# Performance work log

Hardware: AMD Instinct MI355X
Metric: run time of the kernel (lower is better)

## Reference

```python
import jax, jax.numpy as jnp
import numpy as np

N = 131072        # total points
M = 34            # max_num_neighbors (hard-coded in forward)
K = 15            # kernel points (torch-points3d default for 3D KPConv)
C_IN, C_OUT = 32, 64
POINT_INFLUENCE = 0.04        # prev_grid_size * sigma
KERNEL_RADIUS = 1.5 * POINT_INFLUENCE  # _INFLUENCE_TO_RADIUS * point_influence
BN_EPS = 1e-5
NEG_SLOPE = 0.2


def setup_inputs() -> dict:
    key = jax.random.key(0)
    ks = jax.random.split(key, 6)
    # points in a [0, 0.1]^3 box so random neighbors can fall inside the influence radius
    xyz = jax.random.uniform(ks[0], (N, 3), jnp.float32) * 0.1
    feats = jax.random.normal(ks[1], (N, C_IN), jnp.float32)
    neighbor_idx = jax.random.randint(ks[2], (N, M), 0, N, dtype=jnp.int32)
    # fixed kernel-point disposition: points inside a sphere of radius KERNEL_RADIUS
    kp_dir = jax.random.normal(ks[3], (K, 3), jnp.float32)
    kp_dir = kp_dir / jnp.linalg.norm(kp_dir, axis=1, keepdims=True)
    kp_rad = jax.random.uniform(ks[4], (K, 1), jnp.float32) ** (1.0 / 3.0)
    k_points = kp_dir * kp_rad * KERNEL_RADIUS
    weight = jax.random.normal(ks[5], (K, C_IN, C_OUT), jnp.float32) / np.sqrt(K * C_IN)
    gamma = jnp.ones((C_OUT,), jnp.float32)
    beta = jnp.zeros((C_OUT,), jnp.float32)
    return {"xyz": xyz, "feats": feats, "neighbor_idx": neighbor_idx,
            "weight": weight, "k_points": k_points, "gamma": gamma, "beta": beta}


def _kpconv(xyz, feats, neighbor_idx, weight, k_points):
    # shadow point / shadow feature row for out-of-range neighbor index == N
    sup = jnp.concatenate([xyz, jnp.full((1, 3), 1e6, xyz.dtype)], axis=0)
    f = jnp.concatenate([feats, jnp.zeros((1, feats.shape[1]), feats.dtype)], axis=0)
    # [N, M, 3] neighbor offsets relative to each query point
    nb = sup[neighbor_idx] - xyz[:, None, :]
    # [N, M, K] distance from each neighbor to each kernel point
    diff = nb[:, :, None, :] - k_points[None, None, :, :]
    dist = jnp.sqrt(jnp.sum(diff * diff, axis=-1))
    # linear kernel influence, 'sum' aggregation
    w = jnp.maximum(0.0, 1.0 - dist / POINT_INFLUENCE)          # [N, M, K]
    nb_f = f[neighbor_idx]                                       # [N, M, C_IN]
    wf = jnp.einsum('nmk,nmc->nkc', w, nb_f)                     # [N, K, C_IN]
    return jnp.einsum('nkc,kcd->nd', wf, weight)                 # [N, C_OUT]


def reference(xyz, feats, neighbor_idx, weight, k_points, gamma, beta):
    out = _kpconv(xyz, feats, neighbor_idx, weight, k_points)
    # FastBatchNorm1d (training-mode batch statistics) + LeakyReLU(0.2)
    mean = jnp.mean(out, axis=0)
    var = jnp.mean((out - mean) ** 2, axis=0)
    out = (out - mean) * jax.lax.rsqrt(var + BN_EPS) * gamma + beta
    return jnp.where(out >= 0, out, NEG_SLOPE * out)
```

## Files before the change

kernel.cpp:

```cpp
#include <hip/hip_runtime.h>

#define NPTS 131072
#define MNBR 34
#define KP 15
#define CIN 32
#define COUT 64
#define INV_INFL 25.0f
#define BN_EPS 1e-5f
#define NEG_SLOPE 0.2f
#define PPB 16
#define NBLK (NPTS / PPB)
#define NBIN 512

typedef unsigned short u16;
typedef unsigned int u32;
typedef short short8 __attribute__((ext_vector_type(8)));
typedef float f32x4 __attribute__((ext_vector_type(4)));

static __device__ __forceinline__ u16 f2bf(float f) {
    u32 x = __float_as_uint(f);
    x += 0x7fffu + ((x >> 16) & 1u);
    return (u16)(x >> 16);
}
static __device__ __forceinline__ u32 pk2bf(float lo, float hi) {
    u32 a = __float_as_uint(lo) + 0x8000u;
    u32 b = __float_as_uint(hi) + 0x8000u;
    return (a >> 16) | (b & 0xffff0000u);
}

#define WS_WT   0u
#define WS_SCSH 65536u
#define WS_SP   131072u
#define WS_QP   262144u
#define WS_XY   393216u
#define WS_FB   2490624u

__global__ __launch_bounds__(256) void prep(const float* __restrict__ Wg,
                                            const float* __restrict__ feats,
                                            const float* __restrict__ xyz,
                                            u16* __restrict__ WT, float4* __restrict__ XY,
                                            u32* __restrict__ FBu, float* __restrict__ SpQp) {
    int b = blockIdx.x;
    if (b < 120) {
        int i2 = b * 256 + threadIdx.x;
        WT[(i2 & 63) * 480 + (i2 >> 6)] = f2bf(Wg[i2]);
    } else if (b < 633) {
        int r = (b - 120) * 256 + threadIdx.x;
        if (r <= NPTS) {
            float4 v;
            if (r < NPTS) v = make_float4(xyz[3 * r], xyz[3 * r + 1], xyz[3 * r + 2], 0.f);
            else          v = make_float4(1e6f, 1e6f, 1e6f, 0.f);
            XY[r] = v;
        }
    } else if (b < 8826) {
        int g = (b - 633) * 256 + threadIdx.x;
        if (g < ((NPTS + 1) * CIN) / 2) {
            int e = g * 2;
            u32 v = 0;
            if (e < NPTS * CIN)
                v = (u32)f2bf(feats[e]) | ((u32)f2bf(feats[e + 1]) << 16);
            FBu[g] = v;
        }
    } else {
        SpQp[(b - 8826) * 256 + threadIdx.x] = 0.f;
    }
}

__global__ __launch_bounds__(128, 3) void kpconv_conv(
    const float* __restrict__ xyz, const int* __restrict__ nbr,
    const float4* __restrict__ XY, const u32* __restrict__ FBu,
    const u16* __restrict__ WT, const float* __restrict__ kpts,
    float* __restrict__ out, float* __restrict__ Sp, float* __restrict__ Qp)
{
    __shared__ u32 wf[PPB * 256];
    __shared__ float4 offs4[2][2][64];
    __shared__ u32 idxs[2][2][64];

    const int tid = threadIdx.x, lane = tid & 63, wave = tid >> 6;
    const int q = lane >> 4, t = lane & 15;
    const int pbase = blockIdx.x * PPB + wave * 8;

    float axt = 0.f, ayt = 0.f, azt = 0.f, ckt = 1e30f;
    if (t < KP) {
        float kx = kpts[3 * t], ky = kpts[3 * t + 1], kz = kpts[3 * t + 2];
        axt = -2.f * kx; ayt = -2.f * ky; azt = -2.f * kz;
        ckt = fmaf(kx, kx, fmaf(ky, ky, kz * kz));
    }
    const int wslot = (lane & ~7) | ((lane ^ (lane >> 3)) & 7);

    auto ldnbr = [&](int pp) {
        int v = NPTS;
        if (lane < MNBR) v = nbr[(size_t)(pbase + pp) * MNBR + lane];
        if ((u32)v > (u32)NPTS) v = NPTS;
        return v;
    };

    u32 fbC[8], fbN[8] = {0,0,0,0,0,0,0,0};
    u32 d32C = 0, d33C = 0, d32N = 0, d33N = 0;

    int ixA = ldnbr(0);
    int ix1 = ldnbr(1);
    int ix2 = ldnbr(2);
    float4 pn0 = XY[ixA];
    float4 pn1 = XY[ix1];
    {
        const int n1 = pbase;
        float qx = xyz[3 * n1], qy = xyz[3 * n1 + 1], qz = xyz[3 * n1 + 2];
        float ox = pn0.x - qx, oy = pn0.y - qy, oz = pn0.z - qz;
        offs4[wave][0][wslot] = make_float4(ox, oy, oz, fmaf(ox, ox, fmaf(oy, oy, oz * oz)));
        idxs[wave][0][lane] = (u32)ixA;
        #pragma unroll
        for (int j = 0; j < 8; ++j) {
            u32 row = idxs[wave][0][q * 8 + j];
            fbC[j] = FBu[(size_t)row * 16 + t];
        }
        int r32 = __builtin_amdgcn_readlane(ixA, 32);
        int r33 = __builtin_amdgcn_readlane(ixA, 33);
        d32C = FBu[(size_t)r32 * 16 + t];
        d33C = FBu[(size_t)r33 * 16 + t];
    }

    for (int p = 0; p < 8; ++p) {
        int ixN = NPTS;
        if (p < 5) ixN = ldnbr(p + 3);
        float4 pn2 = make_float4(1e6f, 1e6f, 1e6f, 0.f);
        if (p < 6) pn2 = XY[ix2];
        if (p < 7) {
            const int n1 = pbase + p + 1;
            float qx = xyz[3 * n1], qy = xyz[3 * n1 + 1], qz = xyz[3 * n1 + 2];
            float ox = pn1.x - qx, oy = pn1.y - qy, oz = pn1.z - qz;
            const int bb = (p + 1) & 1;
            offs4[wave][bb][wslot] = make_float4(ox, oy, oz, fmaf(ox, ox, fmaf(oy, oy, oz * oz)));
            idxs[wave][bb][lane] = (u32)ix1;
            #pragma unroll
            for (int j = 0; j < 8; ++j) {
                u32 row = idxs[wave][bb][q * 8 + j];
                fbN[j] = FBu[(size_t)row * 16 + t];
            }
            int r32 = __builtin_amdgcn_readlane(ix1, 32);
            int r33 = __builtin_amdgcn_readlane(ix1, 33);
            d32N = FBu[(size_t)r32 * 16 + t];
            d33N = FBu[(size_t)r33 * 16 + t];
        }

        const float4* ob = &offs4[wave][p & 1][0];
        float wj[8];
        #pragma unroll
        for (int j = 0; j < 8; ++j) {
            float4 o = ob[q * 8 + (j ^ q)];
            float d2 = fmaf(o.x, axt, fmaf(o.y, ayt, fmaf(o.z, azt, ckt))) + o.w;
            float dd = __builtin_amdgcn_sqrtf(d2);
            wj[j] = fmaxf(0.f, fmaf(dd, -INV_INFL, 1.f));
        }
        union { short8 v; u32 d[4]; } a1, a2, e1, o1, e2, o2;
        #pragma unroll
        for (int i = 0; i < 4; ++i) a1.d[i] = pk2bf(wj[2 * i], wj[2 * i + 1]);
        {
            float4 oA = ob[36], oB = ob[37];
            float dA = __builtin_amdgcn_sqrtf(fmaf(oA.x, axt, fmaf(oA.y, ayt, fmaf(oA.z, azt, ckt))) + oA.w);
            float dB = __builtin_amdgcn_sqrtf(fmaf(oB.x, axt, fmaf(oB.y, ayt, fmaf(oB.z, azt, ckt))) + oB.w);
            float wA = fmaxf(0.f, fmaf(dA, -INV_INFL, 1.f));
            float wB = fmaxf(0.f, fmaf(dB, -INV_INFL, 1.f));
            a2.d[0] = (q == 0) ? pk2bf(wA, wB) : 0u;
            a2.d[1] = 0; a2.d[2] = 0; a2.d[3] = 0;
        }
        #pragma unroll
        for (int i = 0; i < 4; ++i) {
            u32 aa = fbC[2 * i], bb2 = fbC[2 * i + 1];
            e1.d[i] = (aa & 0xffffu) | (bb2 << 16);
            o1.d[i] = (aa >> 16) | (bb2 & 0xffff0000u);
        }
        {
            u32 lo = (d32C & 0xffffu) | (d33C << 16);
            u32 hi = (d32C >> 16) | (d33C & 0xffff0000u);
            e2.d[0] = (q == 0) ? lo : 0u;  e2.d[1] = 0; e2.d[2] = 0; e2.d[3] = 0;
            o2.d[0] = (q == 0) ? hi : 0u;  o2.d[1] = 0; o2.d[2] = 0; o2.d[3] = 0;
        }
        f32x4 c0 = {0.f, 0.f, 0.f, 0.f}, c1 = {0.f, 0.f, 0.f, 0.f};
        c0 = __builtin_amdgcn_mfma_f32_16x16x32_bf16(a1.v, e1.v, c0, 0, 0, 0);
        c0 = __builtin_amdgcn_mfma_f32_16x16x32_bf16(a2.v, e2.v, c0, 0, 0, 0);
        c1 = __builtin_amdgcn_mfma_f32_16x16x32_bf16(a1.v, o1.v, c1, 0, 0, 0);
        c1 = __builtin_amdgcn_mfma_f32_16x16x32_bf16(a2.v, o2.v, c1, 0, 0, 0);

        const int row = wave * 8 + p;
        #pragma unroll
        for (int r = 0; r < 4; ++r) {
            int ko = q * 4 + r;
            u32 pk = pk2bf(c0[r], c1[r]);
            int unit = ko * 4 + (t >> 2);
            wf[row * 256 + ((unit ^ (row & 7)) << 2) + (t & 3)] = pk;
        }

        #pragma unroll
        for (int j = 0; j < 8; ++j) fbC[j] = fbN[j];
        d32C = d32N; d33C = d33N;
        pn1 = pn2; ix1 = ix2; ix2 = ixN;
    }
    __syncthreads();

    const int wcol0 = (wave * 2 + 0) * 16 + t;
    const int wcol1 = (wave * 2 + 1) * 16 + t;
    f32x4 A0 = {0.f, 0.f, 0.f, 0.f}, A1 = {0.f, 0.f, 0.f, 0.f};
    const u16* wt0 = WT + wcol0 * 480 + q * 8;
    const u16* wt1 = WT + wcol1 * 480 + q * 8;
    #pragma unroll
    for (int ks = 0; ks < KP; ++ks) {
        const int u = ks * 4 + q;
        short8 a   = *(const short8*)&wf[t * 256 + ((u ^ (t & 7)) << 2)];
        short8 bb0 = *(const short8*)(wt0 + ks * 32);
        short8 bb1 = *(const short8*)(wt1 + ks * 32);
        A0 = __builtin_amdgcn_mfma_f32_16x16x32_bf16(a, bb0, A0, 0, 0, 0);
        A1 = __builtin_amdgcn_mfma_f32_16x16x32_bf16(a, bb1, A1, 0, 0, 0);
    }
    const int base = blockIdx.x * PPB;
    float s0 = 0.f, q0 = 0.f, s1 = 0.f, q1 = 0.f;
    #pragma unroll
    for (int r = 0; r < 4; ++r) {
        float v0 = A0[r], v1 = A1[r];
        out[(base + q * 4 + r) * COUT + wcol0] = v0;
        out[(base + q * 4 + r) * COUT + wcol1] = v1;
        s0 += v0; q0 = fmaf(v0, v0, q0);
        s1 += v1; q1 = fmaf(v1, v1, q1);
    }
    s0 += __shfl_xor(s0, 16, 64); s0 += __shfl_xor(s0, 32, 64);
    q0 += __shfl_xor(q0, 16, 64); q0 += __shfl_xor(q0, 32, 64);
    s1 += __shfl_xor(s1, 16, 64); s1 += __shfl_xor(s1, 32, 64);
    q1 += __shfl_xor(q1, 16, 64); q1 += __shfl_xor(q1, 32, 64);
    if (q == 0) {
        const int bin = blockIdx.x >> 4;
        atomicAdd(&Sp[wcol0 * NBIN + bin], s0);
        atomicAdd(&Qp[wcol0 * NBIN + bin], q0);
        atomicAdd(&Sp[wcol1 * NBIN + bin], s1);
        atomicAdd(&Qp[wcol1 * NBIN + bin], q1);
    }
}

__global__ __launch_bounds__(256) void bn_reduce(
    const float* __restrict__ Sp, const float* __restrict__ Qp,
    const float* __restrict__ gamma, const float* __restrict__ beta,
    float* __restrict__ scsh)
{
    const int ch = blockIdx.x;
    const int tid = threadIdx.x;
    float s = 0.f, qq = 0.f;
    if (tid < NBIN / 4) {
        float4 a = ((const float4*)(Sp + ch * NBIN))[tid]; s  = a.x + a.y + a.z + a.w;
        float4 b = ((const float4*)(Qp + ch * NBIN))[tid]; qq = b.x + b.y + b.z + b.w;
    }
    #pragma unroll
    for (int off = 1; off < 64; off <<= 1) {
        s += __shfl_xor(s, off, 64); qq += __shfl_xor(qq, off, 64);
    }
    __shared__ float red[8];
    const int w = tid >> 6;
    if ((tid & 63) == 0) { red[w * 2] = s; red[w * 2 + 1] = qq; }
    __syncthreads();
    if (tid == 0) {
        s  = red[0] + red[2] + red[4] + red[6];
        qq = red[1] + red[3] + red[5] + red[7];
        float mean = s * (1.0f / NPTS);
        float var  = qq * (1.0f / NPTS) - mean * mean;
        float sc = gamma[ch] * rsqrtf(var + BN_EPS);
        scsh[ch] = sc;
        scsh[64 + ch] = beta[ch] - mean * sc;
    }
}

__global__ __launch_bounds__(256) void bn_apply(
    float* __restrict__ out, const float* __restrict__ scsh)
{
    __shared__ float sc[64], sh[64];
    const int tid = threadIdx.x;
    if (tid < 64) { sc[tid] = scsh[tid]; sh[tid] = scsh[64 + tid]; }
    __syncthreads();
    const int gid = blockIdx.x * 256 + tid;
    float4 v = ((const float4*)out)[gid];
    const int c0 = (gid * 4) & 63;
    float y0 = fmaf(v.x, sc[c0 + 0], sh[c0 + 0]);
    float y1 = fmaf(v.y, sc[c0 + 1], sh[c0 + 1]);
    float y2 = fmaf(v.z, sc[c0 + 2], sh[c0 + 2]);
    float y3 = fmaf(v.w, sc[c0 + 3], sh[c0 + 3]);
    float4 w;
    w.x = fmaxf(y0, NEG_SLOPE * y0);
    w.y = fmaxf(y1, NEG_SLOPE * y1);
    w.z = fmaxf(y2, NEG_SLOPE * y2);
    w.w = fmaxf(y3, NEG_SLOPE * y3);
    ((float4*)out)[gid] = w;
}

extern "C" void kernel_launch(void* const* d_in, const int* in_sizes, int n_in,
                              void* d_out, int out_size, void* d_ws, size_t ws_size,
                              hipStream_t stream) {
    (void)in_sizes; (void)n_in; (void)out_size; (void)ws_size;
    const float* xyz   = (const float*)d_in[0];
    const float* feats = (const float*)d_in[1];
    const int*   nbr   = (const int*)d_in[2];
    const float* Wg    = (const float*)d_in[3];
    const float* kpts  = (const float*)d_in[4];
    const float* gamma = (const float*)d_in[5];
    const float* beta  = (const float*)d_in[6];
    float* out = (float*)d_out;
    char* ws = (char*)d_ws;
    u16*    WT   = (u16*)(ws + WS_WT);
    float*  scsh = (float*)(ws + WS_SCSH);
    float*  Sp   = (float*)(ws + WS_SP);
    float*  Qp   = (float*)(ws + WS_QP);
    float4* XY   = (float4*)(ws + WS_XY);
    u32*    FBu  = (u32*)(ws + WS_FB);

    prep<<<dim3(9082), dim3(256), 0, stream>>>(Wg, feats, xyz, WT, XY, FBu, Sp);
    kpconv_conv<<<dim3(NBLK), dim3(128), 0, stream>>>(xyz, nbr, XY, FBu, WT, kpts, out, Sp, Qp);
    bn_reduce<<<dim3(64), dim3(256), 0, stream>>>(Sp, Qp, gamma, beta, scsh);
    bn_apply<<<dim3((NPTS * COUT) / (256 * 4)), dim3(256), 0, stream>>>(out, scsh);
}
```

Measured before the change: 219.9 us.

## Replace LDS staging with wave shuffles and deepen feature prefetch pipeline

Drops the shared-memory offset and index staging buffers and instead broadcasts neighbor offsets and indices across lanes with __shfl and readlane. Feature gathers now run two points ahead instead of one, the point loop is fully unrolled, bf16 packing uses v_perm, and launch bounds are raised to 5 blocks per CU. The goal is to remove LDS round-trips and hide more gather latency. In exchange it needs more registers for the extra prefetch stage while the tighter launch bound caps register use, which may cause spills, and it adds many shuffle instructions.

```diff
diff --git a/kernel.cpp b/kernel.cpp
--- a/kernel.cpp
+++ b/kernel.cpp
@@ -66,18 +66,17 @@
     }
 }
 
-__global__ __launch_bounds__(128, 3) void kpconv_conv(
+__global__ __launch_bounds__(128, 5) void kpconv_conv(
     const float* __restrict__ xyz, const int* __restrict__ nbr,
     const float4* __restrict__ XY, const u32* __restrict__ FBu,
     const u16* __restrict__ WT, const float* __restrict__ kpts,
     float* __restrict__ out, float* __restrict__ Sp, float* __restrict__ Qp)
 {
     __shared__ u32 wf[PPB * 256];
-    __shared__ float4 offs4[2][2][64];
-    __shared__ u32 idxs[2][2][64];
 
     const int tid = threadIdx.x, lane = tid & 63, wave = tid >> 6;
     const int q = lane >> 4, t = lane & 15;
+    const int q8 = q * 8;
     const int pbase = blockIdx.x * PPB + wave * 8;
 
     float axt = 0.f, ayt = 0.f, azt = 0.f, ckt = 1e30f;
@@ -86,7 +85,6 @@
         axt = -2.f * kx; ayt = -2.f * ky; azt = -2.f * kz;
         ckt = fmaf(kx, kx, fmaf(ky, ky, kz * kz));
     }
-    const int wslot = (lane & ~7) | ((lane ^ (lane >> 3)) & 7);
 
     auto ldnbr = [&](int pp) {
         int v = NPTS;
@@ -94,61 +92,48 @@
         if ((u32)v > (u32)NPTS) v = NPTS;
         return v;
     };
-
-    u32 fbC[8], fbN[8] = {0,0,0,0,0,0,0,0};
-    u32 d32C = 0, d33C = 0, d32N = 0, d33N = 0;
-
-    int ixA = ldnbr(0);
-    int ix1 = ldnbr(1);
-    int ix2 = ldnbr(2);
-    float4 pn0 = XY[ixA];
+    auto ldfb = [&](int ix, u32* fb, u32& d32, u32& d33) {
+        #pragma unroll
+        for (int j = 0; j < 8; ++j) {
+            int rj = __shfl(ix, q8 + j, 64);
+            fb[j] = FBu[(size_t)rj * 16 + t];
+        }
+        int r32 = __builtin_amdgcn_readlane(ix, 32);
+        int r33 = __builtin_amdgcn_readlane(ix, 33);
+        d32 = FBu[(size_t)r32 * 16 + t];
+        d33 = FBu[(size_t)r33 * 16 + t];
+    };
+
+    int ixC = ldnbr(0), ix1 = ldnbr(1), ix2 = ldnbr(2);
+    float4 pnC = XY[ixC];
     float4 pn1 = XY[ix1];
-    {
-        const int n1 = pbase;
-        float qx = xyz[3 * n1], qy = xyz[3 * n1 + 1], qz = xyz[3 * n1 + 2];
-        float ox = pn0.x - qx, oy = pn0.y - qy, oz = pn0.z - qz;
-        offs4[wave][0][wslot] = make_float4(ox, oy, oz, fmaf(ox, ox, fmaf(oy, oy, oz * oz)));
-        idxs[wave][0][lane] = (u32)ixA;
-        #pragma unroll
-        for (int j = 0; j < 8; ++j) {
-            u32 row = idxs[wave][0][q * 8 + j];
-            fbC[j] = FBu[(size_t)row * 16 + t];
-        }
-        int r32 = __builtin_amdgcn_readlane(ixA, 32);
-        int r33 = __builtin_amdgcn_readlane(ixA, 33);
-        d32C = FBu[(size_t)r32 * 16 + t];
-        d33C = FBu[(size_t)r33 * 16 + t];
-    }
-
+    u32 fbC[8], fb1[8], fb2[8];
+    u32 d32C, d33C, d32_1, d33_1, d32_2, d33_2;
+    ldfb(ixC, fbC, d32C, d33C);
+    ldfb(ix1, fb1, d32_1, d33_1);
+
+    #pragma unroll
     for (int p = 0; p < 8; ++p) {
         int ixN = NPTS;
         if (p < 5) ixN = ldnbr(p + 3);
         float4 pn2 = make_float4(1e6f, 1e6f, 1e6f, 0.f);
         if (p < 6) pn2 = XY[ix2];
-        if (p < 7) {
-            const int n1 = pbase + p + 1;
-            float qx = xyz[3 * n1], qy = xyz[3 * n1 + 1], qz = xyz[3 * n1 + 2];
-            float ox = pn1.x - qx, oy = pn1.y - qy, oz = pn1.z - qz;
-            const int bb = (p + 1) & 1;
-            offs4[wave][bb][wslot] = make_float4(ox, oy, oz, fmaf(ox, ox, fmaf(oy, oy, oz * oz)));
-            idxs[wave][bb][lane] = (u32)ix1;
-            #pragma unroll
-            for (int j = 0; j < 8; ++j) {
-                u32 row = idxs[wave][bb][q * 8 + j];
-                fbN[j] = FBu[(size_t)row * 16 + t];
-            }
-            int r32 = __builtin_amdgcn_readlane(ix1, 32);
-            int r33 = __builtin_amdgcn_readlane(ix1, 33);
-            d32N = FBu[(size_t)r32 * 16 + t];
-            d33N = FBu[(size_t)r33 * 16 + t];
-        }
-
-        const float4* ob = &offs4[wave][p & 1][0];
+        if (p < 6) ldfb(ix2, fb2, d32_2, d33_2);
+        else { d32_2 = 0; d33_2 = 0; }
+
+        const int n = pbase + p;
+        const float qx = xyz[3 * n], qy = xyz[3 * n + 1], qz = xyz[3 * n + 2];
+        float ox = pnC.x - qx, oy = pnC.y - qy, oz = pnC.z - qz;
+        const float oo = fmaf(ox, ox, fmaf(oy, oy, oz * oz));
+
         float wj[8];
         #pragma unroll
         for (int j = 0; j < 8; ++j) {
-            float4 o = ob[q * 8 + (j ^ q)];
-            float d2 = fmaf(o.x, axt, fmaf(o.y, ayt, fmaf(o.z, azt, ckt))) + o.w;
+            float oxj = __shfl(ox, q8 + j, 64);
+            float oyj = __shfl(oy, q8 + j, 64);
+            float ozj = __shfl(oz, q8 + j, 64);
+            float ooj = __shfl(oo, q8 + j, 64);
+            float d2 = fmaf(oxj, axt, fmaf(oyj, ayt, fmaf(ozj, azt, ckt))) + ooj;
             float dd = __builtin_amdgcn_sqrtf(d2);
             wj[j] = fmaxf(0.f, fmaf(dd, -INV_INFL, 1.f));
         }
@@ -156,9 +141,16 @@
         #pragma unroll
         for (int i = 0; i < 4; ++i) a1.d[i] = pk2bf(wj[2 * i], wj[2 * i + 1]);
         {
-            float4 oA = ob[36], oB = ob[37];
-            float dA = __builtin_amdgcn_sqrtf(fmaf(oA.x, axt, fmaf(oA.y, ayt, fmaf(oA.z, azt, ckt))) + oA.w);
-            float dB = __builtin_amdgcn_sqrtf(fmaf(oB.x, axt, fmaf(oB.y, ayt, fmaf(oB.z, azt, ckt))) + oB.w);
+            float oxA = __uint_as_float(__builtin_amdgcn_readlane(__float_as_uint(ox), 32));
+            float oyA = __uint_as_float(__builtin_amdgcn_readlane(__float_as_uint(oy), 32));
+            float ozA = __uint_as_float(__builtin_amdgcn_readlane(__float_as_uint(oz), 32));
+            float ooA = __uint_as_float(__builtin_amdgcn_readlane(__float_as_uint(oo), 32));
+            float oxB = __uint_as_float(__builtin_amdgcn_readlane(__float_as_uint(ox), 33));
+            float oyB = __uint_as_float(__builtin_amdgcn_readlane(__float_as_uint(oy), 33));
+            float ozB = __uint_as_float(__builtin_amdgcn_readlane(__float_as_uint(oz), 33));
+            float ooB = __uint_as_float(__builtin_amdgcn_readlane(__float_as_uint(oo), 33));
+            float dA = __builtin_amdgcn_sqrtf(fmaf(oxA, axt, fmaf(oyA, ayt, fmaf(ozA, azt, ckt))) + ooA);
+            float dB = __builtin_amdgcn_sqrtf(fmaf(oxB, axt, fmaf(oyB, ayt, fmaf(ozB, azt, ckt))) + ooB);
             float wA = fmaxf(0.f, fmaf(dA, -INV_INFL, 1.f));
             float wB = fmaxf(0.f, fmaf(dB, -INV_INFL, 1.f));
             a2.d[0] = (q == 0) ? pk2bf(wA, wB) : 0u;
@@ -167,12 +159,12 @@
         #pragma unroll
         for (int i = 0; i < 4; ++i) {
             u32 aa = fbC[2 * i], bb2 = fbC[2 * i + 1];
-            e1.d[i] = (aa & 0xffffu) | (bb2 << 16);
-            o1.d[i] = (aa >> 16) | (bb2 & 0xffff0000u);
+            e1.d[i] = __builtin_amdgcn_perm(bb2, aa, 0x05040100u);
+            o1.d[i] = __builtin_amdgcn_perm(bb2, aa, 0x07060302u);
         }
         {
-            u32 lo = (d32C & 0xffffu) | (d33C << 16);
-            u32 hi = (d32C >> 16) | (d33C & 0xffff0000u);
+            u32 lo = __builtin_amdgcn_perm(d33C, d32C, 0x05040100u);
+            u32 hi = __builtin_amdgcn_perm(d33C, d32C, 0x07060302u);
             e2.d[0] = (q == 0) ? lo : 0u;  e2.d[1] = 0; e2.d[2] = 0; e2.d[3] = 0;
             o2.d[0] = (q == 0) ? hi : 0u;  o2.d[1] = 0; o2.d[2] = 0; o2.d[3] = 0;
         }
@@ -191,10 +183,11 @@
             wf[row * 256 + ((unit ^ (row & 7)) << 2) + (t & 3)] = pk;
         }
 
-        #pragma unroll
-        for (int j = 0; j < 8; ++j) fbC[j] = fbN[j];
-        d32C = d32N; d33C = d33N;
-        pn1 = pn2; ix1 = ix2; ix2 = ixN;
+        pnC = pn1; pn1 = pn2;
+        ixC = ix1; ix1 = ix2; ix2 = ixN;
+        #pragma unroll
+        for (int j = 0; j < 8; ++j) { fbC[j] = fb1[j]; fb1[j] = fb2[j]; }
+        d32C = d32_1; d33C = d33_1; d32_1 = d32_2; d33_1 = d33_2;
     }
     __syncthreads();
 
```

After: 220.7 us. Within noise of the previous version (+0.4%).
